# Performance work log

Measured on AMD Instinct MI355X. Metric: run time of the kernel, lower is better.

The kernel has to match this reference:

```python
import jax, jax.numpy as jnp
import numpy as np

B, S, H, I, NH, E = 16, 512, 1024, 4096, 16, 8
DH = H // NH
EPS = 1e-12


def layer_norm(x, g, b):
    mu = jnp.mean(x, axis=-1, keepdims=True)
    var = jnp.mean(jnp.square(x - mu), axis=-1, keepdims=True)
    return (x - mu) * jax.lax.rsqrt(var + EPS) * g + b


def setup_inputs() -> dict:
    key = jax.random.key(0)
    ks = jax.random.split(key, 16)
    s_h = 1.0 / np.sqrt(H)
    s_i = 1.0 / np.sqrt(I)
    return {
        "hidden_states": jax.random.normal(ks[0], (B, S, H), jnp.float32),
        "Wq": jax.random.normal(ks[1], (H, H), jnp.float32) * s_h,
        "bq": jnp.zeros((H,), jnp.float32),
        "Wk": jax.random.normal(ks[2], (H, H), jnp.float32) * s_h,
        "bk": jnp.zeros((H,), jnp.float32),
        "Wv": jax.random.normal(ks[3], (H, H), jnp.float32) * s_h,
        "bv": jnp.zeros((H,), jnp.float32),
        "Wo": jax.random.normal(ks[4], (H, H), jnp.float32) * s_h,
        "bo": jnp.zeros((H,), jnp.float32),
        "ln1_g": jnp.ones((H,), jnp.float32),
        "ln1_b": jnp.zeros((H,), jnp.float32),
        "ln2_g": jnp.ones((H,), jnp.float32),
        "ln2_b": jnp.zeros((H,), jnp.float32),
        "gate_W": jax.random.normal(ks[5], (H, E), jnp.float32) * s_h,
        "W_up": jax.random.normal(ks[6], (E, H, I), jnp.float32) * s_h,
        "b_up": jnp.zeros((E, I), jnp.float32),
        "W_down": jax.random.normal(ks[7], (E, I, H), jnp.float32) * s_i,
        "b_down": jnp.zeros((E, H), jnp.float32),
    }


def reference(hidden_states, Wq, bq, Wk, bk, Wv, bv, Wo, bo,
              ln1_g, ln1_b, ln2_g, ln2_b, gate_W, W_up, b_up, W_down, b_down):
    x = hidden_states
    # --- BERT self-attention ---
    q = (x @ Wq + bq).reshape(B, S, NH, DH)
    k = (x @ Wk + bk).reshape(B, S, NH, DH)
    v = (x @ Wv + bv).reshape(B, S, NH, DH)
    scores = jnp.einsum("bqhd,bkhd->bhqk", q, k) / np.sqrt(DH)
    probs = jax.nn.softmax(scores, axis=-1)
    ctx = jnp.einsum("bhqk,bkhd->bqhd", probs, v).reshape(B, S, H)
    # BertSelfOutput: dense + residual + LayerNorm
    attn_out = layer_norm(ctx @ Wo + bo + x, ln1_g, ln1_b)

    # --- feed_forward_chunk: pre-LN, MoE, residual (residual on attn_out) ---
    x_ln = layer_norm(attn_out, ln2_g, ln2_b)
    router_output = jnp.einsum("bsh,he->bse", x_ln, gate_W)
    router_logits = jnp.mean(router_output, axis=1)          # [B, E]
    choice = jnp.argmax(router_logits, axis=-1)              # softmax-argmax == logits-argmax

    # per-sample top-1 expert: gather each sample's expert weights, batched GEMM
    Wu = W_up[choice]                                        # [B, H, I]
    Wd = W_down[choice]                                      # [B, I, H]
    h = jax.nn.gelu(jnp.einsum("bsh,bhi->bsi", x_ln, Wu) + b_up[choice][:, None, :],
                    approximate=False)
    moe = jnp.einsum("bsi,bih->bsh", h, Wd) + b_down[choice][:, None, :]
    layer_output = moe + attn_out
    return (layer_output, router_logits)
```

## Files before the change

kernel.cpp:

```cpp
#include <hip/hip_runtime.h>


typedef __attribute__((ext_vector_type(4))) float f32x4;
typedef __attribute__((ext_vector_type(8))) short s8v;
typedef __attribute__((ext_vector_type(4))) short s4v;
typedef unsigned short u16;

#define DEV static __device__ __forceinline__

DEV u16 f2bf(float f){
  union { float f; unsigned u; } v; v.f = f;
  unsigned r = v.u + 0x7fffu + ((v.u >> 16) & 1u);
  return (u16)(r >> 16);
}

DEV f32x4 mfma16(s8v a, s8v b, f32x4 c){
  return __builtin_amdgcn_mfma_f32_16x16x32_bf16(a, b, c, 0, 0, 0);
}

DEV float wave_sum(float s){
#pragma unroll
  for (int o = 1; o < 64; o <<= 1) s += __shfl_xor(s, o);
  return s;
}

#define ASYNC_COPY16(g, l) \
  __builtin_amdgcn_global_load_lds((const __attribute__((address_space(1))) void*)(g), \
                                   (__attribute__((address_space(3))) void*)(l), 16, 0, 0)

__global__ __launch_bounds__(256) void cvt_bf16(const float* __restrict__ in,
                                                u16* __restrict__ out)
{
  const size_t i = ((size_t)blockIdx.x * 256 + threadIdx.x) * 8;
  f32x4 a = *(const f32x4*)&in[i];
  f32x4 b = *(const f32x4*)&in[i + 4];
  s8v o;
#pragma unroll
  for (int j = 0; j < 4; ++j){ o[j] = (short)f2bf(a[j]); o[4 + j] = (short)f2bf(b[j]); }
  *(s8v*)&out[i] = o;
}

__global__ __launch_bounds__(256) void transpose_w(const float* __restrict__ in,
                                                   u16* __restrict__ out, int R, int C)
{
  __shared__ float t[64][65];
  const size_t bs = (size_t)blockIdx.z * R * (size_t)C;
  in += bs; out += bs;
  const int c0 = blockIdx.x * 64, r0 = blockIdx.y * 64;
  const int tx = threadIdx.x & 63, ty = threadIdx.x >> 6;
#pragma unroll
  for (int j = 0; j < 64; j += 4) t[ty + j][tx] = in[(size_t)(r0 + ty + j) * C + c0 + tx];
  __syncthreads();
#pragma unroll
  for (int j = 0; j < 64; j += 4) out[(size_t)(c0 + ty + j) * R + r0 + tx] = f2bf(t[tx][ty + j]);
}

template<int MODE, bool SWZ>
__global__ __launch_bounds__(256, 2) void gemm_bt(
    const u16* __restrict__ A, const u16* __restrict__ Bt,
    const float* __restrict__ bias, void* __restrict__ outp,
    const float* __restrict__ resid, int M, int N, int K,
    const int* __restrict__ choice,
    long aBatch, long outBatch, long residBatch, long btExpert, long biasExpert,
    void* __restrict__ out2, void* __restrict__ out3)
{
  int bx, by, bz;
  if (SWZ){
    const int nx = gridDim.x, ny = gridDim.y;
    const int nwg = nx * ny * gridDim.z;
    int id = blockIdx.x + nx * (blockIdx.y + ny * blockIdx.z);
    if ((nwg & 7) == 0){ const int q = nwg >> 3; id = (id & 7) * q + (id >> 3); }
    bx = id % nx; const int r2 = id / nx; by = r2 % ny; bz = r2 / ny;
  } else {
    bx = blockIdx.x; by = blockIdx.y; bz = blockIdx.z;
  }
  const int z = bz;
  if (choice){
    const int e = choice[z];
    Bt   += (size_t)e * btExpert;
    bias += (size_t)e * biasExpert;
  }
  A += (size_t)z * aBatch;

  const int tid = threadIdx.x;
  const int lane = tid & 63, wid = tid >> 6;
  const int hi = lane >> 4, l15 = lane & 15;
  const int wr = wid >> 1, wc = wid & 1;
  const long row0 = (long)bx * 256;
  const long col0 = (long)by * 128;

  __shared__ __align__(16) u16 lA[3][256 * 32];
  __shared__ __align__(16) u16 lB[3][128 * 32];

  f32x4 acc[8][4];
#pragma unroll
  for (int i = 0; i < 8; ++i)
#pragma unroll
    for (int j = 0; j < 4; ++j) acc[i][j] = f32x4{0.f, 0.f, 0.f, 0.f};

  const int srow = tid >> 2;
  const int scol = (((tid & 3) ^ (srow & 3)) << 3);
  const u16* pA[4]; const u16* pB[2];
#pragma unroll
  for (int j = 0; j < 4; ++j) pA[j] = A  + (row0 + j * 64 + srow) * (size_t)K + scol;
#pragma unroll
  for (int j = 0; j < 2; ++j) pB[j] = Bt + (col0 + j * 64 + srow) * (size_t)K + scol;

#define GSTAGE(S_) do { \
  _Pragma("unroll") \
  for (int j = 0; j < 4; ++j) ASYNC_COPY16(pA[j], &lA[S_][(j * 256 + tid) * 8]); \
  _Pragma("unroll") \
  for (int j = 0; j < 2; ++j) ASYNC_COPY16(pB[j], &lB[S_][(j * 256 + tid) * 8]); \
  _Pragma("unroll") \
  for (int j = 0; j < 4; ++j) pA[j] += 32; \
  _Pragma("unroll") \
  for (int j = 0; j < 2; ++j) pB[j] += 32; \
} while (0)

  const int baseA = (wr * 128 + l15) * 32 + ((hi ^ (l15 & 3)) << 3);
  const int baseB = (wc * 64  + l15) * 32 + ((hi ^ (l15 & 3)) << 3);

#define ITER(S_, S2_, WSTR_, DOSTAGE_) do { \
  asm volatile("s_waitcnt vmcnt(" WSTR_ ")" ::: "memory"); \
  __builtin_amdgcn_s_barrier(); \
  __builtin_amdgcn_sched_barrier(0); \
  asm volatile("" ::: "memory"); \
  if (DOSTAGE_) GSTAGE(S2_); \
  s8v af[8], bfv[4]; \
  _Pragma("unroll") \
  for (int mi = 0; mi < 8; ++mi) af[mi] = *(const s8v*)&lA[S_][baseA + mi * 512]; \
  _Pragma("unroll") \
  for (int ni = 0; ni < 4; ++ni) bfv[ni] = *(const s8v*)&lB[S_][baseB + ni * 512]; \
  __builtin_amdgcn_s_setprio(1); \
  _Pragma("unroll") \
  for (int mi = 0; mi < 8; ++mi) \
    _Pragma("unroll") \
    for (int ni = 0; ni < 4; ++ni) \
      acc[mi][ni] = mfma16(af[mi], bfv[ni], acc[mi][ni]); \
  __builtin_amdgcn_s_setprio(0); \
} while (0)

  const int nk = K >> 5;
  GSTAGE(0); GSTAGE(1);

  for (int t = 0; t < nk - 2; t += 3){
    ITER(0, 2, "6", 1);
    ITER(1, 0, "6", 1);
    ITER(2, 1, "6", 1);
  }
  ITER(0, 0, "6", 0);
  ITER(1, 0, "0", 0);
#undef ITER
#undef GSTAGE

#pragma unroll
  for (int mi = 0; mi < 8; ++mi){
    const long rowb = row0 + wr * 128 + mi * 16 + hi * 4;
#pragma unroll
    for (int ni = 0; ni < 4; ++ni){
      const long col = col0 + wc * 64 + ni * 16 + l15;
      const float bv = bias[col];
#pragma unroll
      for (int r = 0; r < 4; ++r){
        const long row = rowb + r;
        float v = acc[mi][ni][r] + bv;
        if (MODE == 2){
          float* o = (float*)outp + (size_t)z * outBatch;
          const float* rs = resid + (size_t)z * residBatch;
          o[row * N + col] = v + rs[row * N + col];
        } else if (MODE == 1){
          u16* o = (u16*)outp + (size_t)z * outBatch;
          const float gv = 0.5f * v * (1.0f + erff(v * 0.70710678118654752f));
          o[row * N + col] = f2bf(gv);
        } else if (MODE == 4){
          const int seg = (int)(col >> 10), lc = (int)(col & 1023);
          const u16 bv16 = f2bf(v);
          if (seg == 0)      ((u16*)outp)[row * 1024 + lc] = bv16;
          else if (seg == 1) ((u16*)out2)[row * 1024 + lc] = bv16;
          else {
            const int bb = (int)(row >> 9), ss = (int)(row & 511);
            const int hh = lc >> 6, dd = lc & 63;
            ((u16*)out3)[(((size_t)(bb * 16 + hh)) * 64 + dd) * 512 + ss] = bv16;
          }
        }
      }
    }
  }
}

__global__ __launch_bounds__(256) void attn_fwd(
    const u16* __restrict__ qb, const u16* __restrict__ kb,
    const u16* __restrict__ vt, u16* __restrict__ ctx)
{
  const int tid = threadIdx.x;
  const int lane = tid & 63, wid = tid >> 6;
  const int hi = lane >> 4, l15 = lane & 15;
  const int h = blockIdx.y, b = blockIdx.z;
  const int q0 = blockIdx.x * 128 + wid * 32;

  const u16* kp0 = kb + (size_t)b * 512 * 1024 + h * 64;
  const u16* vp0 = vt + ((size_t)(b * 16 + h)) * 64 * 512;

  __shared__ __align__(16) u16 lK[2][64 * 64];
  __shared__ __align__(16) u16 lV[2][64 * 64];
  __shared__ __align__(16) u16 lP[4][2][16][72];

#define STAGE(bsel, k0s) do { \
  _Pragma("unroll") \
  for (int i = 0; i < 2; ++i){ \
    const int idx = i * 256 + tid; \
    const int row = idx >> 3, seg = idx & 7; \
    const int sc = ((seg ^ (row & 7)) << 3); \
    ASYNC_COPY16(kp0 + (size_t)((k0s) + row) * 1024 + sc, &lK[bsel][idx * 8]); \
    ASYNC_COPY16(vp0 + (size_t)row * 512 + (k0s) + sc,    &lV[bsel][idx * 8]); \
  } \
} while (0)

  const u16* qp = qb + ((size_t)b * 512 + q0) * 1024 + h * 64;
  s8v qf[2][2];
#pragma unroll
  for (int qt = 0; qt < 2; ++qt)
#pragma unroll
    for (int st = 0; st < 2; ++st)
      qf[qt][st] = *(const s8v*)&qp[(size_t)(qt * 16 + l15) * 1024 + st * 32 + hi * 8];

  f32x4 o[2][4];
#pragma unroll
  for (int qt = 0; qt < 2; ++qt)
#pragma unroll
    for (int mi = 0; mi < 4; ++mi) o[qt][mi] = f32x4{0.f, 0.f, 0.f, 0.f};
  float mrun[2] = {-3e38f, -3e38f}, lrun[2] = {0.f, 0.f};

  STAGE(0, 0);
  __syncthreads();

  for (int t = 0; t < 8; ++t){
    const int buf = t & 1;
    if (t < 7) STAGE(buf ^ 1, (t + 1) * 64);

    f32x4 s[2][4];
#pragma unroll
    for (int qt = 0; qt < 2; ++qt)
#pragma unroll
      for (int kt = 0; kt < 4; ++kt) s[qt][kt] = f32x4{0.f, 0.f, 0.f, 0.f};
#pragma unroll
    for (int st = 0; st < 2; ++st){
      s8v kf[4];
#pragma unroll
      for (int kt = 0; kt < 4; ++kt){
        const int row = kt * 16 + l15;
        kf[kt] = *(const s8v*)&lK[buf][row * 64 + (((st * 4 + hi) ^ (row & 7)) << 3)];
      }
#pragma unroll
      for (int qt = 0; qt < 2; ++qt)
#pragma unroll
        for (int kt = 0; kt < 4; ++kt)
          s[qt][kt] = mfma16(kf[kt], qf[qt][st], s[qt][kt]);
    }

#pragma unroll
    for (int qt = 0; qt < 2; ++qt){
      float mx = s[qt][0][0];
#pragma unroll
      for (int kt = 0; kt < 4; ++kt)
#pragma unroll
        for (int r = 0; r < 4; ++r) mx = fmaxf(mx, s[qt][kt][r]);
      mx *= 0.125f;
      mx = fmaxf(mx, __shfl_xor(mx, 16));
      mx = fmaxf(mx, __shfl_xor(mx, 32));
      const float mnew = fmaxf(mrun[qt], mx);
      const float alpha = __expf(mrun[qt] - mnew);
      mrun[qt] = mnew;
      float ps = 0.f;
#pragma unroll
      for (int kt = 0; kt < 4; ++kt){
        s4v pk;
#pragma unroll
        for (int r = 0; r < 4; ++r){
          const float p = __expf(s[qt][kt][r] * 0.125f - mnew);
          ps += p; pk[r] = (short)f2bf(p);
        }
        *(s4v*)&lP[wid][qt][l15][kt * 16 + 4 * hi] = pk;
      }
      ps += __shfl_xor(ps, 16);
      ps += __shfl_xor(ps, 32);
      lrun[qt] = lrun[qt] * alpha + ps;
#pragma unroll
      for (int mi = 0; mi < 4; ++mi)
#pragma unroll
        for (int r = 0; r < 4; ++r) o[qt][mi][r] *= alpha;
    }

#pragma unroll
    for (int ks = 0; ks < 2; ++ks){
      s8v vf[4];
#pragma unroll
      for (int mi = 0; mi < 4; ++mi){
        const int row = mi * 16 + l15;
        vf[mi] = *(const s8v*)&lV[buf][row * 64 + (((ks * 4 + hi) ^ (row & 7)) << 3)];
      }
#pragma unroll
      for (int qt = 0; qt < 2; ++qt){
        const s8v pf = *(const s8v*)&lP[wid][qt][l15][ks * 32 + 8 * hi];
#pragma unroll
        for (int mi = 0; mi < 4; ++mi)
          o[qt][mi] = mfma16(vf[mi], pf, o[qt][mi]);
      }
    }
    __syncthreads();
  }
#undef STAGE

#pragma unroll
  for (int qt = 0; qt < 2; ++qt){
    const float inv = 1.f / lrun[qt];
    u16* cp = ctx + ((size_t)b * 512 + q0 + qt * 16 + l15) * 1024 + h * 64;
#pragma unroll
    for (int mi = 0; mi < 4; ++mi)
#pragma unroll
      for (int r = 0; r < 4; ++r)
        cp[mi * 16 + 4 * hi + r] = f2bf(o[qt][mi][r] * inv);
  }
}

__global__ __launch_bounds__(256, 2) void ln12_colsum(
    float* __restrict__ t, const float* __restrict__ g1, const float* __restrict__ b1,
    const float* __restrict__ g2, const float* __restrict__ b2,
    u16* __restrict__ xln, float* __restrict__ colsum)
{
  const int b = blockIdx.y;
  const int wid = threadIdx.x >> 6, lane = threadIdx.x & 63;
  __shared__ float cacc[1024];
  for (int i = threadIdx.x; i < 1024; i += 256) cacc[i] = 0.f;
  __syncthreads();
  float acc[16];
#pragma unroll
  for (int i = 0; i < 16; ++i) acc[i] = 0.f;
  const int rbase = b * 512 + blockIdx.x * 64 + wid * 16;
  for (int rr = 0; rr < 16; ++rr){
    float* p = t + (size_t)(rbase + rr) * 1024;
    f32x4 v[4];
#pragma unroll
    for (int c = 0; c < 4; ++c) v[c] = *(const f32x4*)&p[c * 256 + lane * 4];
    float s = 0.f;
#pragma unroll
    for (int c = 0; c < 4; ++c) s += v[c][0] + v[c][1] + v[c][2] + v[c][3];
    const float mu = wave_sum(s) * (1.f / 1024.f);
    float s2 = 0.f;
#pragma unroll
    for (int c = 0; c < 4; ++c)
#pragma unroll
      for (int j = 0; j < 4; ++j){ const float d = v[c][j] - mu; s2 += d * d; }
    const float rs = rsqrtf(wave_sum(s2) * (1.f / 1024.f) + 1e-12f);
    float y1s = 0.f;
#pragma unroll
    for (int c = 0; c < 4; ++c){
      const f32x4 gg = *(const f32x4*)&g1[c * 256 + lane * 4];
      const f32x4 bb = *(const f32x4*)&b1[c * 256 + lane * 4];
#pragma unroll
      for (int j = 0; j < 4; ++j){
        v[c][j] = (v[c][j] - mu) * rs * gg[j] + bb[j];
        y1s += v[c][j];
      }
      *(f32x4*)&p[c * 256 + lane * 4] = v[c];
    }
    const float mu2 = wave_sum(y1s) * (1.f / 1024.f);
    float s22 = 0.f;
#pragma unroll
    for (int c = 0; c < 4; ++c)
#pragma unroll
      for (int j = 0; j < 4; ++j){ const float d = v[c][j] - mu2; s22 += d * d; }
    const float rs2 = rsqrtf(wave_sum(s22) * (1.f / 1024.f) + 1e-12f);
    u16* op = xln + (size_t)(rbase + rr) * 1024;
#pragma unroll
    for (int c = 0; c < 4; ++c){
      const f32x4 gg = *(const f32x4*)&g2[c * 256 + lane * 4];
      const f32x4 bb = *(const f32x4*)&b2[c * 256 + lane * 4];
      s4v ov;
#pragma unroll
      for (int j = 0; j < 4; ++j){
        const float y = (v[c][j] - mu2) * rs2 * gg[j] + bb[j];
        acc[c * 4 + j] += y;
        ov[j] = (short)f2bf(y);
      }
      *(s4v*)&op[c * 256 + lane * 4] = ov;
    }
  }
#pragma unroll
  for (int c = 0; c < 4; ++c)
#pragma unroll
    for (int j = 0; j < 4; ++j)
      atomicAdd(&cacc[c * 256 + lane * 4 + j], acc[c * 4 + j]);
  __syncthreads();
  for (int i = threadIdx.x; i < 1024; i += 256) atomicAdd(&colsum[b * 1024 + i], cacc[i]);
}

__global__ void router_argmax(const float* __restrict__ colsum, const float* __restrict__ gate,
                              float* __restrict__ logits, int* __restrict__ choice)
{
  const int b = blockIdx.x, lane = threadIdx.x;
  float pa[8];
#pragma unroll
  for (int e = 0; e < 8; ++e) pa[e] = 0.f;
  for (int it = 0; it < 16; ++it){
    const int hh = it * 64 + lane;
    const float c = colsum[b * 1024 + hh];
    const float* gp = gate + (size_t)hh * 8;
#pragma unroll
    for (int e = 0; e < 8; ++e) pa[e] += c * gp[e];
  }
#pragma unroll
  for (int e = 0; e < 8; ++e) pa[e] = wave_sum(pa[e]);
  if (lane == 0){
    float best = -3e38f; int bi = 0;
#pragma unroll
    for (int e = 0; e < 8; ++e){
      const float lg = pa[e] * (1.f / 512.f);
      logits[b * 8 + e] = lg;
      if (lg > best){ best = lg; bi = e; }
    }
    choice[b] = bi;
  }
}

extern "C" void kernel_launch(void* const* d_in, const int* in_sizes, int n_in,
                              void* d_out, int out_size, void* d_ws, size_t ws_size,
                              hipStream_t stream)
{
  const float* x    = (const float*)d_in[0];
  const float* Wq   = (const float*)d_in[1];
  const float* bq   = (const float*)d_in[2];
  const float* Wk   = (const float*)d_in[3];
  const float* bk   = (const float*)d_in[4];
  const float* Wv   = (const float*)d_in[5];
  const float* bv   = (const float*)d_in[6];
  const float* Wo   = (const float*)d_in[7];
  const float* bo   = (const float*)d_in[8];
  const float* ln1g = (const float*)d_in[9];
  const float* ln1b = (const float*)d_in[10];
  const float* ln2g = (const float*)d_in[11];
  const float* ln2b = (const float*)d_in[12];
  const float* gate = (const float*)d_in[13];
  const float* Wup  = (const float*)d_in[14];
  const float* bup  = (const float*)d_in[15];
  const float* Wdn  = (const float*)d_in[16];
  const float* bdn  = (const float*)d_in[17];

  size_t off = 0;
  char* wsb = (char*)d_ws;
  auto take = [&](size_t n) -> void* {
    void* p = wsb + off; off += (n + 255) & ~(size_t)255; return p;
  };
  u16*   x_bf  = (u16*)take(8192ull * 1024 * 2);
  u16*   Wqt   = (u16*)take(1024ull * 1024 * 2);
  u16*   Wkt   = (u16*)take(1024ull * 1024 * 2);
  u16*   Wvt   = (u16*)take(1024ull * 1024 * 2);
  u16*   Wot   = (u16*)take(1024ull * 1024 * 2);
  u16*   q_bf  = (u16*)take(8192ull * 1024 * 2);
  u16*   k_bf  = (u16*)take(8192ull * 1024 * 2);
  u16*   vt_bf = (u16*)take(8192ull * 1024 * 2);
  float* tmp   = (float*)take(8192ull * 1024 * 4);
  u16*   Wupt  = (u16*)take(8ull * 4096 * 1024 * 2);
  u16*   Wdnt  = (u16*)take(8ull * 1024 * 4096 * 2);
  u16*   h_bf  = (u16*)take(8192ull * 4096 * 2);
  float* colsum = (float*)take(16ull * 1024 * 4);
  int*   choice = (int*)take(256);
  float* qkvb  = (float*)take(3072 * 4);

  u16* ctx = x_bf;
  u16* xln = q_bf;
  float* logits = (float*)d_out + 8388608;

  cvt_bf16<<<4096, 256, 0, stream>>>(x, x_bf);
  transpose_w<<<dim3(16, 16, 1), 256, 0, stream>>>(Wq,  Wqt,  1024, 1024);
  transpose_w<<<dim3(16, 16, 1), 256, 0, stream>>>(Wk,  Wkt,  1024, 1024);
  transpose_w<<<dim3(16, 16, 1), 256, 0, stream>>>(Wv,  Wvt,  1024, 1024);
  transpose_w<<<dim3(16, 16, 1), 256, 0, stream>>>(Wo,  Wot,  1024, 1024);
  transpose_w<<<dim3(64, 16, 8), 256, 0, stream>>>(Wup, Wupt, 1024, 4096);
  transpose_w<<<dim3(16, 64, 8), 256, 0, stream>>>(Wdn, Wdnt, 4096, 1024);
  hipMemcpyAsync(qkvb,        bq, 1024 * 4, hipMemcpyDeviceToDevice, stream);
  hipMemcpyAsync(qkvb + 1024, bk, 1024 * 4, hipMemcpyDeviceToDevice, stream);
  hipMemcpyAsync(qkvb + 2048, bv, 1024 * 4, hipMemcpyDeviceToDevice, stream);

  gemm_bt<4, true><<<dim3(32, 24, 1), 256, 0, stream>>>(x_bf, Wqt, qkvb, q_bf,
      nullptr, 8192, 3072, 1024, nullptr, 0, 0, 0, 0, 0, k_bf, vt_bf);

  attn_fwd<<<dim3(4, 16, 16), 256, 0, stream>>>(q_bf, k_bf, vt_bf, ctx);

  gemm_bt<2, true><<<dim3(32, 8, 1), 256, 0, stream>>>(ctx, Wot, bo, tmp, x,
      8192, 1024, 1024, nullptr, 0, 0, 0, 0, 0, nullptr, nullptr);
  hipMemsetAsync(colsum, 0, 16 * 1024 * sizeof(float), stream);
  ln12_colsum<<<dim3(8, 16), 256, 0, stream>>>(tmp, ln1g, ln1b, ln2g, ln2b, xln, colsum);
  router_argmax<<<16, 64, 0, stream>>>(colsum, gate, logits, choice);

  gemm_bt<1, true><<<dim3(2, 32, 16), 256, 0, stream>>>(xln, Wupt, bup, h_bf, nullptr,
      512, 4096, 1024, choice, 512ll * 1024, 512ll * 4096, 0, 4096ll * 1024, 4096,
      nullptr, nullptr);
  gemm_bt<2, true><<<dim3(2, 8, 16), 256, 0, stream>>>(h_bf, Wdnt, bdn, d_out, tmp,
      512, 1024, 4096, choice, 512ll * 4096, 512ll * 1024, 512ll * 1024, 1024ll * 4096, 1024,
      nullptr, nullptr);
}
```

Before: 602.5 us.

## Restructure GEMM to 512 threads, K=64 tiles, split-phase load/MFMA pipeline

The bf16 GEMM now runs 8 waves per block instead of 4, doubles the K step per stage to 64 with an 8-way XOR swizzle, and splits each tile into two half-phases. In each half, LDS reads and async global copies are interleaved with MFMA bursts behind extra barriers. Each wave holds a 64x64 accumulator instead of 128x64, which cuts register pressure and raises the number of waves available to hide latency. In exchange, LDS use doubles to about 144KB for three stages, which may limit occupancy to one block per CU despite the launch bound of two, and the extra barriers add sync overhead.

```diff
diff --git a/kernel.cpp b/kernel.cpp
--- a/kernel.cpp
+++ b/kernel.cpp
@@ -56,7 +56,7 @@
 }
 
 template<int MODE, bool SWZ>
-__global__ __launch_bounds__(256, 2) void gemm_bt(
+__global__ __launch_bounds__(512, 2) void gemm_bt(
     const u16* __restrict__ A, const u16* __restrict__ Bt,
     const float* __restrict__ bias, void* __restrict__ outp,
     const float* __restrict__ resid, int M, int N, int K,
@@ -89,73 +89,112 @@
   const long row0 = (long)bx * 256;
   const long col0 = (long)by * 128;
 
-  __shared__ __align__(16) u16 lA[3][256 * 32];
-  __shared__ __align__(16) u16 lB[3][128 * 32];
-
-  f32x4 acc[8][4];
-#pragma unroll
-  for (int i = 0; i < 8; ++i)
+  __shared__ __align__(16) u16 lA[3][256 * 64];
+  __shared__ __align__(16) u16 lB[3][128 * 64];
+
+  f32x4 acc[4][4];
+#pragma unroll
+  for (int i = 0; i < 4; ++i)
 #pragma unroll
     for (int j = 0; j < 4; ++j) acc[i][j] = f32x4{0.f, 0.f, 0.f, 0.f};
 
-  const int srow = tid >> 2;
-  const int scol = (((tid & 3) ^ (srow & 3)) << 3);
+  const int srow = tid >> 3, sseg = tid & 7;
+  const int scol = ((sseg ^ (srow & 7)) << 3);
   const u16* pA[4]; const u16* pB[2];
 #pragma unroll
   for (int j = 0; j < 4; ++j) pA[j] = A  + (row0 + j * 64 + srow) * (size_t)K + scol;
 #pragma unroll
   for (int j = 0; j < 2; ++j) pB[j] = Bt + (col0 + j * 64 + srow) * (size_t)K + scol;
 
-#define GSTAGE(S_) do { \
-  _Pragma("unroll") \
-  for (int j = 0; j < 4; ++j) ASYNC_COPY16(pA[j], &lA[S_][(j * 256 + tid) * 8]); \
-  _Pragma("unroll") \
-  for (int j = 0; j < 2; ++j) ASYNC_COPY16(pB[j], &lB[S_][(j * 256 + tid) * 8]); \
-  _Pragma("unroll") \
-  for (int j = 0; j < 4; ++j) pA[j] += 32; \
-  _Pragma("unroll") \
-  for (int j = 0; j < 2; ++j) pB[j] += 32; \
+#define STG_A(S_, J_) ASYNC_COPY16(pA[J_], &lA[S_][(J_ * 512 + tid) * 8])
+#define STG_B(S_, J_) ASYNC_COPY16(pB[J_], &lB[S_][(J_ * 512 + tid) * 8])
+#define STG_ADV() do { \
+  _Pragma("unroll") \
+  for (int j = 0; j < 4; ++j) pA[j] += 64; \
+  _Pragma("unroll") \
+  for (int j = 0; j < 2; ++j) pB[j] += 64; \
 } while (0)
 
-  const int baseA = (wr * 128 + l15) * 32 + ((hi ^ (l15 & 3)) << 3);
-  const int baseB = (wc * 64  + l15) * 32 + ((hi ^ (l15 & 3)) << 3);
-
-#define ITER(S_, S2_, WSTR_, DOSTAGE_) do { \
-  asm volatile("s_waitcnt vmcnt(" WSTR_ ")" ::: "memory"); \
+  const int key = l15 & 7;
+  const int sA0 = (hi ^ key) << 3;
+  const int sA1 = ((4 | hi) ^ key) << 3;
+  const int baseAr = (wr * 64 + l15) * 64;
+  const int baseBr = (wc * 64 + l15) * 64;
+
+#define TILE(S_, S2_, VMS_, DOSTG_) do { \
+  asm volatile("s_waitcnt vmcnt(" VMS_ ")" ::: "memory"); \
   __builtin_amdgcn_s_barrier(); \
   __builtin_amdgcn_sched_barrier(0); \
-  asm volatile("" ::: "memory"); \
-  if (DOSTAGE_) GSTAGE(S2_); \
-  s8v af[8], bfv[4]; \
-  _Pragma("unroll") \
-  for (int mi = 0; mi < 8; ++mi) af[mi] = *(const s8v*)&lA[S_][baseA + mi * 512]; \
-  _Pragma("unroll") \
-  for (int ni = 0; ni < 4; ++ni) bfv[ni] = *(const s8v*)&lB[S_][baseB + ni * 512]; \
+  s8v fb[4][2], faL[2][2], faH[2][2]; \
+  _Pragma("unroll") \
+  for (int ni = 0; ni < 4; ++ni){ \
+    fb[ni][0] = *(const s8v*)&lB[S_][baseBr + ni * 1024 + sA0]; \
+    fb[ni][1] = *(const s8v*)&lB[S_][baseBr + ni * 1024 + sA1]; \
+  } \
+  _Pragma("unroll") \
+  for (int mi = 0; mi < 2; ++mi){ \
+    faL[mi][0] = *(const s8v*)&lA[S_][baseAr + mi * 1024 + sA0]; \
+    faL[mi][1] = *(const s8v*)&lA[S_][baseAr + mi * 1024 + sA1]; \
+  } \
+  if (DOSTG_){ STG_A(S2_, 0); STG_A(S2_, 1); STG_B(S2_, 0); } \
+  __builtin_amdgcn_s_barrier(); \
+  asm volatile("s_waitcnt lgkmcnt(0)" ::: "memory"); \
+  __builtin_amdgcn_sched_barrier(0); \
   __builtin_amdgcn_s_setprio(1); \
   _Pragma("unroll") \
-  for (int mi = 0; mi < 8; ++mi) \
+  for (int mi = 0; mi < 2; ++mi) \
     _Pragma("unroll") \
     for (int ni = 0; ni < 4; ++ni) \
-      acc[mi][ni] = mfma16(af[mi], bfv[ni], acc[mi][ni]); \
+      acc[mi][ni] = mfma16(faL[mi][1], fb[ni][1], \
+                    mfma16(faL[mi][0], fb[ni][0], acc[mi][ni])); \
+  __builtin_amdgcn_s_setprio(0); \
+  __builtin_amdgcn_s_barrier(); \
+  _Pragma("unroll") \
+  for (int mi = 0; mi < 2; ++mi){ \
+    faH[mi][0] = *(const s8v*)&lA[S_][baseAr + (mi + 2) * 1024 + sA0]; \
+    faH[mi][1] = *(const s8v*)&lA[S_][baseAr + (mi + 2) * 1024 + sA1]; \
+  } \
+  if (DOSTG_){ STG_A(S2_, 2); STG_A(S2_, 3); STG_B(S2_, 1); STG_ADV(); } \
+  __builtin_amdgcn_s_barrier(); \
+  asm volatile("s_waitcnt lgkmcnt(0)" ::: "memory"); \
+  __builtin_amdgcn_sched_barrier(0); \
+  __builtin_amdgcn_s_setprio(1); \
+  _Pragma("unroll") \
+  for (int mi = 0; mi < 2; ++mi) \
+    _Pragma("unroll") \
+    for (int ni = 0; ni < 4; ++ni) \
+      acc[mi + 2][ni] = mfma16(faH[mi][1], fb[ni][1], \
+                        mfma16(faH[mi][0], fb[ni][0], acc[mi + 2][ni])); \
   __builtin_amdgcn_s_setprio(0); \
 } while (0)
 
-  const int nk = K >> 5;
-  GSTAGE(0); GSTAGE(1);
-
-  for (int t = 0; t < nk - 2; t += 3){
-    ITER(0, 2, "6", 1);
-    ITER(1, 0, "6", 1);
-    ITER(2, 1, "6", 1);
-  }
-  ITER(0, 0, "6", 0);
-  ITER(1, 0, "0", 0);
-#undef ITER
-#undef GSTAGE
-
-#pragma unroll
-  for (int mi = 0; mi < 8; ++mi){
-    const long rowb = row0 + wr * 128 + mi * 16 + hi * 4;
+  const int nk = K >> 6;
+#pragma unroll
+  for (int j = 0; j < 4; ++j) STG_A(0, j);
+#pragma unroll
+  for (int j = 0; j < 2; ++j) STG_B(0, j);
+  STG_ADV();
+#pragma unroll
+  for (int j = 0; j < 4; ++j) STG_A(1, j);
+#pragma unroll
+  for (int j = 0; j < 2; ++j) STG_B(1, j);
+  STG_ADV();
+
+  for (int t = 0; t < nk - 3; t += 3){
+    const bool stg3 = (t + 4 < nk);
+    TILE(0, 2, "6", 1);
+    TILE(1, 0, "6", 1);
+    TILE(2, 1, "6", stg3);
+  }
+  TILE(0, 0, "0", 0);
+#undef TILE
+#undef STG_A
+#undef STG_B
+#undef STG_ADV
+
+#pragma unroll
+  for (int mi = 0; mi < 4; ++mi){
+    const long rowb = row0 + wr * 64 + mi * 16 + hi * 4;
 #pragma unroll
     for (int ni = 0; ni < 4; ++ni){
       const long col = col0 + wc * 64 + ni * 16 + l15;
@@ -482,21 +521,21 @@
   hipMemcpyAsync(qkvb + 1024, bk, 1024 * 4, hipMemcpyDeviceToDevice, stream);
   hipMemcpyAsync(qkvb + 2048, bv, 1024 * 4, hipMemcpyDeviceToDevice, stream);
 
-  gemm_bt<4, true><<<dim3(32, 24, 1), 256, 0, stream>>>(x_bf, Wqt, qkvb, q_bf,
+  gemm_bt<4, true><<<dim3(32, 24, 1), 512, 0, stream>>>(x_bf, Wqt, qkvb, q_bf,
       nullptr, 8192, 3072, 1024, nullptr, 0, 0, 0, 0, 0, k_bf, vt_bf);
 
   attn_fwd<<<dim3(4, 16, 16), 256, 0, stream>>>(q_bf, k_bf, vt_bf, ctx);
 
-  gemm_bt<2, true><<<dim3(32, 8, 1), 256, 0, stream>>>(ctx, Wot, bo, tmp, x,
+  gemm_bt<2, true><<<dim3(32, 8, 1), 512, 0, stream>>>(ctx, Wot, bo, tmp, x,
       8192, 1024, 1024, nullptr, 0, 0, 0, 0, 0, nullptr, nullptr);
   hipMemsetAsync(colsum, 0, 16 * 1024 * sizeof(float), stream);
   ln12_colsum<<<dim3(8, 16), 256, 0, stream>>>(tmp, ln1g, ln1b, ln2g, ln2b, xln, colsum);
   router_argmax<<<16, 64, 0, stream>>>(colsum, gate, logits, choice);
 
-  gemm_bt<1, true><<<dim3(2, 32, 16), 256, 0, stream>>>(xln, Wupt, bup, h_bf, nullptr,
+  gemm_bt<1, true><<<dim3(2, 32, 16), 512, 0, stream>>>(xln, Wupt, bup, h_bf, nullptr,
       512, 4096, 1024, choice, 512ll * 1024, 512ll * 4096, 0, 4096ll * 1024, 4096,
       nullptr, nullptr);
-  gemm_bt<2, true><<<dim3(2, 8, 16), 256, 0, stream>>>(h_bf, Wdnt, bdn, d_out, tmp,
+  gemm_bt<2, true><<<dim3(2, 8, 16), 512, 0, stream>>>(h_bf, Wdnt, bdn, d_out, tmp,
       512, 1024, 4096, choice, 512ll * 4096, 512ll * 1024, 512ll * 1024, 1024ll * 4096, 1024,
       nullptr, nullptr);
 }
```

Result: faster. 582.2 us (-3.4%).

## Restructure GEMM to 512-thread 256-wide tiles with BK=64 phased double buffering

Applied to the files above, without the earlier changes.

Rewrites the bf16 MFMA GEMM to use 8 waves per block, a 256-column tile, a templated row tile (256 or 128) and a K step of 64. Loads are double buffered with an 8-way XOR swizzle, and global stages are split into phases that interleave with the MFMA work. B fragments are kept in registers across phases. The aim is more data reuse per block and finer overlap of loads with compute. The cost is more LDS use and register pressure, and fewer blocks for the smaller MoE GEMMs.

```diff
diff --git a/kernel.cpp b/kernel.cpp
--- a/kernel.cpp
+++ b/kernel.cpp
@@ -55,8 +55,8 @@
   for (int j = 0; j < 64; j += 4) out[(size_t)(c0 + ty + j) * R + r0 + tx] = f2bf(t[tx][ty + j]);
 }
 
-template<int MODE, bool SWZ>
-__global__ __launch_bounds__(256, 2) void gemm_bt(
+template<int BM, int MODE, bool SWZ>
+__global__ __launch_bounds__(512, 2) void gemm_bt(
     const u16* __restrict__ A, const u16* __restrict__ Bt,
     const float* __restrict__ bias, void* __restrict__ outp,
     const float* __restrict__ resid, int M, int N, int K,
@@ -64,6 +64,9 @@
     long aBatch, long outBatch, long residBatch, long btExpert, long biasExpert,
     void* __restrict__ out2, void* __restrict__ out3)
 {
+  constexpr int MI = BM / 32;
+  constexpr int JA = BM / 64;
+
   int bx, by, bz;
   if (SWZ){
     const int nx = gridDim.x, ny = gridDim.y;
@@ -85,77 +88,116 @@
   const int tid = threadIdx.x;
   const int lane = tid & 63, wid = tid >> 6;
   const int hi = lane >> 4, l15 = lane & 15;
-  const int wr = wid >> 1, wc = wid & 1;
-  const long row0 = (long)bx * 256;
-  const long col0 = (long)by * 128;
-
-  __shared__ __align__(16) u16 lA[3][256 * 32];
-  __shared__ __align__(16) u16 lB[3][128 * 32];
-
-  f32x4 acc[8][4];
-#pragma unroll
-  for (int i = 0; i < 8; ++i)
+  const int wr = wid >> 2, wc = wid & 3;
+  const int keyv = l15 & 7;
+  const long row0 = (long)bx * BM;
+  const long col0 = (long)by * 256;
+
+  __shared__ __align__(16) u16 lA[2][BM * 64];
+  __shared__ __align__(16) u16 lB[2][256 * 64];
+
+  f32x4 acc[MI][4];
+#pragma unroll
+  for (int i = 0; i < MI; ++i)
 #pragma unroll
     for (int j = 0; j < 4; ++j) acc[i][j] = f32x4{0.f, 0.f, 0.f, 0.f};
 
-  const int srow = tid >> 2;
-  const int scol = (((tid & 3) ^ (srow & 3)) << 3);
-  const u16* pA[4]; const u16* pB[2];
-#pragma unroll
-  for (int j = 0; j < 4; ++j) pA[j] = A  + (row0 + j * 64 + srow) * (size_t)K + scol;
-#pragma unroll
-  for (int j = 0; j < 2; ++j) pB[j] = Bt + (col0 + j * 64 + srow) * (size_t)K + scol;
-
-#define GSTAGE(S_) do { \
+  const int srow = tid >> 3;
+  const int scol = (((tid & 7) ^ (srow & 7)) << 3);
+  const u16* pA[4]; const u16* pB[4];
+#pragma unroll
+  for (int j = 0; j < JA; ++j) pA[j] = A  + (row0 + j * 64 + srow) * (size_t)K + scol;
+#pragma unroll
+  for (int j = 0; j < 4; ++j)  pB[j] = Bt + (col0 + j * 64 + srow) * (size_t)K + scol;
+
+#define STGA(S_, J_) ASYNC_COPY16(pA[J_], &lA[S_][((J_) * 512 + tid) * 8])
+#define STGB(S_, J_) ASYNC_COPY16(pB[J_], &lB[S_][((J_) * 512 + tid) * 8])
+#define STG_ADV() do { \
   _Pragma("unroll") \
-  for (int j = 0; j < 4; ++j) ASYNC_COPY16(pA[j], &lA[S_][(j * 256 + tid) * 8]); \
+  for (int j = 0; j < JA; ++j) pA[j] += 64; \
   _Pragma("unroll") \
-  for (int j = 0; j < 2; ++j) ASYNC_COPY16(pB[j], &lB[S_][(j * 256 + tid) * 8]); \
-  _Pragma("unroll") \
-  for (int j = 0; j < 4; ++j) pA[j] += 32; \
-  _Pragma("unroll") \
-  for (int j = 0; j < 2; ++j) pB[j] += 32; \
+  for (int j = 0; j < 4; ++j)  pB[j] += 64; \
 } while (0)
 
-  const int baseA = (wr * 128 + l15) * 32 + ((hi ^ (l15 & 3)) << 3);
-  const int baseB = (wc * 64  + l15) * 32 + ((hi ^ (l15 & 3)) << 3);
-
-#define ITER(S_, S2_, WSTR_, DOSTAGE_) do { \
-  asm volatile("s_waitcnt vmcnt(" WSTR_ ")" ::: "memory"); \
+  s8v fb[4][2];
+
+#define PH(B_, P_, VMS_, ...) do { \
+  asm volatile("s_waitcnt vmcnt(" VMS_ ")" ::: "memory"); \
   __builtin_amdgcn_s_barrier(); \
   __builtin_amdgcn_sched_barrier(0); \
-  asm volatile("" ::: "memory"); \
-  if (DOSTAGE_) GSTAGE(S2_); \
-  s8v af[8], bfv[4]; \
+  if ((P_) == 0){ \
+    _Pragma("unroll") \
+    for (int ni = 0; ni < 4; ++ni) \
+      _Pragma("unroll") \
+      for (int ks = 0; ks < 2; ++ks) \
+        fb[ni][ks] = *(const s8v*)&lB[B_][(wc * 64 + ni * 16 + l15) * 64 \
+                                          + (((ks * 4 + hi) ^ keyv) << 3)]; \
+  } \
+  s8v af[2][2]; \
   _Pragma("unroll") \
-  for (int mi = 0; mi < 8; ++mi) af[mi] = *(const s8v*)&lA[S_][baseA + mi * 512]; \
-  _Pragma("unroll") \
-  for (int ni = 0; ni < 4; ++ni) bfv[ni] = *(const s8v*)&lB[S_][baseB + ni * 512]; \
+  for (int i = 0; i < 2; ++i) \
+    _Pragma("unroll") \
+    for (int ks = 0; ks < 2; ++ks) \
+      af[i][ks] = *(const s8v*)&lA[B_][((2 * (P_) + i) * 32 + wr * 16 + l15) * 64 \
+                                        + (((ks * 4 + hi) ^ keyv) << 3)]; \
+  __VA_ARGS__ \
+  asm volatile("s_waitcnt lgkmcnt(0)" ::: "memory"); \
+  __builtin_amdgcn_sched_barrier(0); \
   __builtin_amdgcn_s_setprio(1); \
   _Pragma("unroll") \
-  for (int mi = 0; mi < 8; ++mi) \
+  for (int i = 0; i < 2; ++i) \
     _Pragma("unroll") \
     for (int ni = 0; ni < 4; ++ni) \
-      acc[mi][ni] = mfma16(af[mi], bfv[ni], acc[mi][ni]); \
+      acc[2 * (P_) + i][ni] = mfma16(af[i][1], fb[ni][1], \
+                              mfma16(af[i][0], fb[ni][0], acc[2 * (P_) + i][ni])); \
   __builtin_amdgcn_s_setprio(0); \
 } while (0)
 
-  const int nk = K >> 5;
-  GSTAGE(0); GSTAGE(1);
-
-  for (int t = 0; t < nk - 2; t += 3){
-    ITER(0, 2, "6", 1);
-    ITER(1, 0, "6", 1);
-    ITER(2, 1, "6", 1);
-  }
-  ITER(0, 0, "6", 0);
-  ITER(1, 0, "0", 0);
-#undef ITER
-#undef GSTAGE
-
-#pragma unroll
-  for (int mi = 0; mi < 8; ++mi){
-    const long rowb = row0 + wr * 128 + mi * 16 + hi * 4;
+  const int nk = K >> 6;
+  STGB(0, 0); STGB(0, 1); STGB(0, 2); STGB(0, 3);
+#pragma unroll
+  for (int j = 0; j < JA; ++j) STGA(0, j);
+  STG_ADV();
+
+  if constexpr (BM == 128){
+    for (int t = 0; t + 2 < nk; t += 2){
+      PH(0, 0, "1", STGB(1, 0); STGB(1, 1); STGB(1, 2););
+      PH(0, 1, "3", STGB(1, 3); STGA(1, 0); STGA(1, 1); STG_ADV(););
+      PH(1, 0, "1", STGB(0, 0); STGB(0, 1); STGB(0, 2););
+      PH(1, 1, "3", STGB(0, 3); STGA(0, 0); STGA(0, 1); STG_ADV(););
+    }
+    PH(0, 0, "1", STGB(1, 0); STGB(1, 1); STGB(1, 2););
+    PH(0, 1, "3", STGB(1, 3); STGA(1, 0); STGA(1, 1););
+    PH(1, 0, "1", );
+    PH(1, 1, "0", );
+  } else {
+    for (int t = 0; t + 2 < nk; t += 2){
+      PH(0, 0, "3", STGB(1, 0); STGB(1, 1););
+      PH(0, 1, "4", STGB(1, 2); STGB(1, 3););
+      PH(0, 2, "5", STGA(1, 0); STGA(1, 1););
+      PH(0, 3, "6", STGA(1, 2); STGA(1, 3); STG_ADV(););
+      PH(1, 0, "3", STGB(0, 0); STGB(0, 1););
+      PH(1, 1, "4", STGB(0, 2); STGB(0, 3););
+      PH(1, 2, "5", STGA(0, 0); STGA(0, 1););
+      PH(1, 3, "6", STGA(0, 2); STGA(0, 3); STG_ADV(););
+    }
+    PH(0, 0, "3", STGB(1, 0); STGB(1, 1););
+    PH(0, 1, "4", STGB(1, 2); STGB(1, 3););
+    PH(0, 2, "5", STGA(1, 0); STGA(1, 1););
+    PH(0, 3, "6", STGA(1, 2); STGA(1, 3););
+    PH(1, 0, "3", );
+    PH(1, 1, "2", );
+    PH(1, 2, "1", );
+    PH(1, 3, "0", );
+  }
+#undef PH
+#undef STGA
+#undef STGB
+#undef STG_ADV
+
+#pragma unroll
+  for (int mi = 0; mi < MI; ++mi){
+    const long rowb = row0 + mi * 32 + wr * 16 + hi * 4;
 #pragma unroll
     for (int ni = 0; ni < 4; ++ni){
       const long col = col0 + wc * 64 + ni * 16 + l15;
@@ -482,21 +524,21 @@
   hipMemcpyAsync(qkvb + 1024, bk, 1024 * 4, hipMemcpyDeviceToDevice, stream);
   hipMemcpyAsync(qkvb + 2048, bv, 1024 * 4, hipMemcpyDeviceToDevice, stream);
 
-  gemm_bt<4, true><<<dim3(32, 24, 1), 256, 0, stream>>>(x_bf, Wqt, qkvb, q_bf,
+  gemm_bt<256, 4, true><<<dim3(32, 12, 1), 512, 0, stream>>>(x_bf, Wqt, qkvb, q_bf,
       nullptr, 8192, 3072, 1024, nullptr, 0, 0, 0, 0, 0, k_bf, vt_bf);
 
   attn_fwd<<<dim3(4, 16, 16), 256, 0, stream>>>(q_bf, k_bf, vt_bf, ctx);
 
-  gemm_bt<2, true><<<dim3(32, 8, 1), 256, 0, stream>>>(ctx, Wot, bo, tmp, x,
+  gemm_bt<128, 2, true><<<dim3(64, 4, 1), 512, 0, stream>>>(ctx, Wot, bo, tmp, x,
       8192, 1024, 1024, nullptr, 0, 0, 0, 0, 0, nullptr, nullptr);
   hipMemsetAsync(colsum, 0, 16 * 1024 * sizeof(float), stream);
   ln12_colsum<<<dim3(8, 16), 256, 0, stream>>>(tmp, ln1g, ln1b, ln2g, ln2b, xln, colsum);
   router_argmax<<<16, 64, 0, stream>>>(colsum, gate, logits, choice);
 
-  gemm_bt<1, true><<<dim3(2, 32, 16), 256, 0, stream>>>(xln, Wupt, bup, h_bf, nullptr,
+  gemm_bt<256, 1, true><<<dim3(2, 16, 16), 512, 0, stream>>>(xln, Wupt, bup, h_bf, nullptr,
       512, 4096, 1024, choice, 512ll * 1024, 512ll * 4096, 0, 4096ll * 1024, 4096,
       nullptr, nullptr);
-  gemm_bt<2, true><<<dim3(2, 8, 16), 256, 0, stream>>>(h_bf, Wdnt, bdn, d_out, tmp,
+  gemm_bt<128, 2, true><<<dim3(4, 4, 16), 512, 0, stream>>>(h_bf, Wdnt, bdn, d_out, tmp,
       512, 1024, 4096, choice, 512ll * 4096, 512ll * 1024, 512ll * 1024, 1024ll * 4096, 1024,
       nullptr, nullptr);
 }
```

Result: faster. 582.6 us (-3.3%).
